# Performance work log

Hardware: AMD Instinct MI355X
Metric: run time of the kernel (lower is better)

## Reference

```python
import jax, jax.numpy as jnp
import numpy as np

DIM = 2560
HEADS = 64
HEAD_DIM = 40
TEMB = 512
FF = 4 * DIM
B = 1
S = 1248
TXT = 224
EPS = 1e-6


def _ln(x, eps=EPS):
    # LayerNorm over last dim, no affine (elementwise_affine=False)
    m = jnp.mean(x, axis=-1, keepdims=True)
    v = jnp.mean(jnp.square(x - m), axis=-1, keepdims=True)
    return (x - m) * jax.lax.rsqrt(v + eps)


def setup_inputs() -> dict:
    key = jax.random.key(0)
    ks = jax.random.split(key, 10)
    w = 0.02
    return {
        "hidden_states": jax.random.normal(ks[0], (B, S, DIM), jnp.float32),
        "emb": jax.random.normal(ks[1], (B, TEMB), jnp.float32),
        "attention_mask": jnp.zeros((B, 1, S, S), jnp.float32),
        "adaln_w": jax.random.normal(ks[2], (TEMB, 12 * DIM), jnp.float32) * w,
        "adaln_b": jnp.zeros((12 * DIM,), jnp.float32),
        "qkv_w": jax.random.normal(ks[3], (DIM, 3 * DIM), jnp.float32) * w,
        "qkv_b": jnp.zeros((3 * DIM,), jnp.float32),
        "out_w": jax.random.normal(ks[4], (DIM, DIM), jnp.float32) * w,
        "out_b": jnp.zeros((DIM,), jnp.float32),
        "ff1_w": jax.random.normal(ks[5], (DIM, FF), jnp.float32) * w,
        "ff1_b": jnp.zeros((FF,), jnp.float32),
        "ff2_w": jax.random.normal(ks[6], (FF, DIM), jnp.float32) * w,
        "ff2_b": jnp.zeros((DIM,), jnp.float32),
        "text_length": TXT,
    }


def reference(hidden_states, emb, attention_mask, adaln_w, adaln_b, qkv_w, qkv_b,
              out_w, out_b, ff1_w, ff1_b, ff2_w, ff2_b, text_length):
    b, s, d = hidden_states.shape
    t = text_length

    # adaLN: SiLU -> Linear(time_embed_dim, 12*dim), chunk into 12 [B, dim] pieces
    ada = jax.nn.silu(emb) @ adaln_w + adaln_b
    (sh_msa_i, sc_msa_i, g_msa_i, sh_mlp_i, sc_mlp_i, g_mlp_i,
     sh_msa_t, sc_msa_t, g_msa_t, sh_mlp_t, sc_mlp_t, g_mlp_t) = jnp.split(ada, 12, axis=1)

    def mod(x, shift, scale):
        return x * (1.0 + scale[:, None, :]) + shift[:, None, :]

    # --- attention block ---
    ai = _ln(hidden_states)
    ai = jnp.concatenate([mod(ai[:, :t], sh_msa_t, sc_msa_t),
                          mod(ai[:, t:], sh_msa_i, sc_msa_i)], axis=1)

    qkv = ai @ qkv_w + qkv_b                              # [B, S, 3*D]
    q, k, v = jnp.split(qkv, 3, axis=-1)
    q = q.reshape(b, s, HEADS, HEAD_DIM).transpose(0, 2, 1, 3)  # [B, H, S, hd]
    k = k.reshape(b, s, HEADS, HEAD_DIM).transpose(0, 2, 1, 3)
    v = v.reshape(b, s, HEADS, HEAD_DIM).transpose(0, 2, 1, 3)

    q = _ln(q)  # per-head QK layernorm
    k = _ln(k)

    scores = jnp.einsum("bhqd,bhkd->bhqk", q, k) / (HEAD_DIM ** 0.5)
    scores = scores + attention_mask
    probs = jax.nn.softmax(scores, axis=-1)
    ctx = jnp.einsum("bhqk,bhkd->bhqd", probs, v)
    ctx = ctx.transpose(0, 2, 1, 3).reshape(b, s, d)
    attn_out = ctx @ out_w + out_b

    h = jnp.concatenate([hidden_states[:, :t] + g_msa_t[:, None, :] * attn_out[:, :t],
                         hidden_states[:, t:] + g_msa_i[:, None, :] * attn_out[:, t:]], axis=1)

    # --- MLP block ---
    mi = _ln(h)
    mi = jnp.concatenate([mod(mi[:, :t], sh_mlp_t, sc_mlp_t),
                          mod(mi[:, t:], sh_mlp_i, sc_mlp_i)], axis=1)
    mo = jax.nn.gelu(mi @ ff1_w + ff1_b, approximate=True) @ ff2_w + ff2_b

    h = jnp.concatenate([h[:, :t] + g_mlp_t[:, None, :] * mo[:, :t],
                         h[:, t:] + g_mlp_i[:, None, :] * mo[:, t:]], axis=1)
    return h
```

## Files before the change

### kernel.cpp

```cpp
#include <hip/hip_runtime.h>
#include <cstdint>

typedef float f32x4 __attribute__((ext_vector_type(4)));
typedef __bf16 bf16x8 __attribute__((ext_vector_type(8)));
typedef __bf16 bf16x4 __attribute__((ext_vector_type(4)));

#define S_LEN 1248
#define S_PAD 1280
#define DIMD 2560
#define NHEAD 64
#define HDIM 40
#define T3 7680

__device__ __forceinline__ f32x4 mfma16(bf16x8 a, bf16x8 b, f32x4 c) {
  return __builtin_amdgcn_mfma_f32_16x16x32_bf16(a, b, c, 0, 0, 0);
}

__global__ void k_adaln(const float* __restrict__ emb, const float* __restrict__ W,
                        const float* __restrict__ b, float* __restrict__ ada) {
  __shared__ __attribute__((aligned(16))) float se[512];
  int tid = threadIdx.x;
  for (int i = tid; i < 512; i += 64) {
    float e = emb[i];
    se[i] = e / (1.f + __expf(-e));
  }
  __syncthreads();
  int col = blockIdx.x * 64 + tid;
  float acc = 0.f;
  #pragma unroll 8
  for (int k = 0; k < 512; ++k) acc += se[k] * W[(size_t)k * 30720 + col];
  ada[col] = acc + b[col];
}

__global__ __launch_bounds__(256) void k_trans(const float* __restrict__ W,
                                               __bf16* __restrict__ Wt, int K, int N) {
  __shared__ __attribute__((aligned(16))) float t[64][65];
  int k0 = blockIdx.y * 64, n0 = blockIdx.x * 64;
  int tid = threadIdx.x;
  #pragma unroll
  for (int i = 0; i < 4; ++i) {
    int r = i * 16 + (tid >> 4), c = (tid & 15) * 4;
    const float4 v = *(const float4*)&W[(size_t)(k0 + r) * N + n0 + c];
    t[r][c] = v.x; t[r][c + 1] = v.y; t[r][c + 2] = v.z; t[r][c + 3] = v.w;
  }
  __syncthreads();
  #pragma unroll
  for (int j = 0; j < 4; ++j) {
    int n = j * 16 + (tid >> 4), kk = (tid & 15) * 4;
    bf16x4 o;
    o[0] = (__bf16)t[kk][n];     o[1] = (__bf16)t[kk + 1][n];
    o[2] = (__bf16)t[kk + 2][n]; o[3] = (__bf16)t[kk + 3][n];
    *(bf16x4*)&Wt[(size_t)(n0 + n) * K + k0 + kk] = o;
  }
}

__global__ __launch_bounds__(256) void k_lnmod(const float* __restrict__ X,
                                               const float* __restrict__ ada,
                                               int csh_t, int csc_t, int csh_i, int csc_i,
                                               const int* __restrict__ tlp,
                                               __bf16* __restrict__ Y) {
  int row = blockIdx.x, tid = threadIdx.x;
  const float* x = X + (size_t)row * DIMD;
  float v[10], s = 0.f, s2 = 0.f;
  #pragma unroll
  for (int i = 0; i < 10; ++i) { v[i] = x[tid + i * 256]; s += v[i]; s2 += v[i] * v[i]; }
  #pragma unroll
  for (int m = 1; m < 64; m <<= 1) { s += __shfl_xor(s, m, 64); s2 += __shfl_xor(s2, m, 64); }
  __shared__ float rs[4], rq[4];
  if ((tid & 63) == 0) { rs[tid >> 6] = s; rq[tid >> 6] = s2; }
  __syncthreads();
  s = rs[0] + rs[1] + rs[2] + rs[3];
  s2 = rq[0] + rq[1] + rq[2] + rq[3];
  float mean = s * (1.f / DIMD);
  float rstd = rsqrtf(s2 * (1.f / DIMD) - mean * mean + 1e-6f);
  int txt = *tlp;
  int csh = row < txt ? csh_t : csh_i, csc = row < txt ? csc_t : csc_i;
  #pragma unroll
  for (int i = 0; i < 10; ++i) {
    int col = tid + i * 256;
    float y = (v[i] - mean) * rstd;
    y = y * (1.f + ada[csc * DIMD + col]) + ada[csh * DIMD + col];
    Y[(size_t)row * DIMD + col] = (__bf16)y;
  }
}

template <int EPI>
__global__ __launch_bounds__(256) void k_gemm(
    const __bf16* __restrict__ A, int lda, const __bf16* __restrict__ Bt, int ldb,
    const float* __restrict__ bias, int N, int ksize,
    float* __restrict__ Cf, float* __restrict__ Cp, __bf16* __restrict__ Cb) {
  __shared__ __attribute__((aligned(16))) __bf16 smem[3][2][4096];
  int tid = threadIdx.x;

  unsigned gx = gridDim.x, gy = gridDim.y;
  unsigned nwg = gx * gy * gridDim.z;
  unsigned orig = (blockIdx.z * gy + blockIdx.y) * gx + blockIdx.x;
  unsigned qq = nwg >> 3, r8 = nwg & 7;
  unsigned xcd = orig & 7, loc = orig >> 3;
  unsigned swz = (xcd < r8 ? xcd * (qq + 1) : r8 * (qq + 1) + (xcd - r8) * qq) + loc;
  unsigned bx = swz % gx;
  unsigned rest = swz / gx;
  unsigned by = rest % gy;
  unsigned bz = rest / gy;

  int m0 = bx * 128, n0 = by * 128;
  int kbase = bz * ksize;
  int wave = tid >> 6, lane = tid & 63;
  int wm = (wave & 1) * 64, wn = (wave >> 1) * 64;
  int l15 = lane & 15, l4 = lane >> 4;
  f32x4 acc[4][4] = {};

  auto STG = [&](__bf16* As, __bf16* Bs, int kk) {
    #pragma unroll
    for (int i = 0; i < 2; ++i) {
      int c = tid + i * 256;
      int row = c >> 2, ko = (c & 3) * 8;
      __builtin_amdgcn_global_load_lds(
          (const __attribute__((address_space(1))) unsigned int*)(A + (size_t)(m0 + row) * lda + kk + ko),
          (__attribute__((address_space(3))) unsigned int*)(As + c * 8), 16, 0, 0);
      __builtin_amdgcn_global_load_lds(
          (const __attribute__((address_space(1))) unsigned int*)(Bt + (size_t)(n0 + row) * ldb + kk + ko),
          (__attribute__((address_space(3))) unsigned int*)(Bs + c * 8), 16, 0, 0);
    }
  };

  int nt = ksize >> 5;
  STG(smem[0][0], smem[0][1], kbase);
  STG(smem[1][0], smem[1][1], kbase + 32);
  asm volatile("s_waitcnt vmcnt(4)" ::: "memory");
  __builtin_amdgcn_s_barrier();

  int rb = 0, sb = 2;
  for (int t = 0; t < nt; ++t) {
    if (t + 2 < nt) STG(smem[sb][0], smem[sb][1], kbase + (t + 2) * 32);
    const __bf16* As = smem[rb][0];
    const __bf16* Bs = smem[rb][1];
    bf16x8 af[4], bfr[4];
    #pragma unroll
    for (int s = 0; s < 4; ++s) {
      af[s] = *(const bf16x8*)&As[(wm + s * 16 + l15) * 32 + l4 * 8];
      bfr[s] = *(const bf16x8*)&Bs[(wn + s * 16 + l15) * 32 + l4 * 8];
    }
    __builtin_amdgcn_s_setprio(1);
    #pragma unroll
    for (int i = 0; i < 4; ++i)
      #pragma unroll
      for (int j = 0; j < 4; ++j)
        acc[i][j] = mfma16(af[i], bfr[j], acc[i][j]);
    __builtin_amdgcn_s_setprio(0);
    __builtin_amdgcn_sched_barrier(0);
    if (t + 2 < nt)
      asm volatile("s_waitcnt vmcnt(4)" ::: "memory");
    else
      asm volatile("s_waitcnt vmcnt(0)" ::: "memory");
    __builtin_amdgcn_s_barrier();
    rb = rb == 2 ? 0 : rb + 1;
    sb = sb == 2 ? 0 : sb + 1;
  }

  float* Cfo = Cf;
  if constexpr (EPI == 3) Cfo = (bz == 0) ? Cf : (Cp + (size_t)(bz - 1) * S_PAD * N);
  #pragma unroll
  for (int i = 0; i < 4; ++i) {
    #pragma unroll
    for (int r = 0; r < 4; ++r) {
      int rr = m0 + wm + i * 16 + l4 * 4 + r;
      if (rr >= S_LEN) continue;
      #pragma unroll
      for (int j = 0; j < 4; ++j) {
        int col = n0 + wn + j * 16 + l15;
        if constexpr (EPI == 0) {
          Cfo[(size_t)rr * N + col] = acc[i][j][r] + bias[col];
        } else if constexpr (EPI == 3) {
          Cfo[(size_t)rr * N + col] = acc[i][j][r];
        } else {
          float val = acc[i][j][r] + bias[col];
          float u = val + 0.044715f * val * val * val;
          float gl = 0.5f * val * (1.f + tanhf(0.7978845608028654f * u));
          Cb[(size_t)rr * N + col] = (__bf16)gl;
        }
      }
    }
  }
}

__global__ __launch_bounds__(256) void k_redq(const float* __restrict__ part,
                                              const float* __restrict__ bias,
                                              float* __restrict__ io) {
  int idx = blockIdx.x * 256 + threadIdx.x;
  int perRow = T3 >> 2;
  int row = idx / perRow;
  int c4 = (idx - row * perRow) << 2;
  size_t off = (size_t)row * T3 + c4;
  const float4 a = *(const float4*)&io[off];
  const float4 p = *(const float4*)&part[off];
  const float4 b = *(const float4*)&bias[c4];
  float4 o;
  o.x = a.x + p.x + b.x; o.y = a.y + p.y + b.y;
  o.z = a.z + p.z + b.z; o.w = a.w + p.w + b.w;
  *(float4*)&io[off] = o;
}

template <int NS>
__global__ __launch_bounds__(256) void k_red(const float* __restrict__ part,
                                             const float* __restrict__ bias,
                                             const float* __restrict__ resid,
                                             const float* __restrict__ ada,
                                             int g_t, int g_i, const int* __restrict__ tlp,
                                             int N, float* __restrict__ out) {
  int idx = blockIdx.x * 256 + threadIdx.x;
  int perRow = N >> 2;
  int row = idx / perRow;
  int c4 = (idx - row * perRow) << 2;
  if (row >= S_LEN) return;
  int txt = *tlp;
  size_t off = (size_t)row * N + c4;
  float4 s = *(const float4*)&part[off];
  #pragma unroll
  for (int z = 1; z < NS; ++z) {
    const float4 p = *(const float4*)&part[(size_t)z * S_PAD * N + off];
    s.x += p.x; s.y += p.y; s.z += p.z; s.w += p.w;
  }
  const float4 bb = *(const float4*)&bias[c4];
  const float4 rr = *(const float4*)&resid[off];
  const float4 gg = *(const float4*)&ada[(size_t)(row < txt ? g_t : g_i) * DIMD + c4];
  float4 o;
  o.x = rr.x + gg.x * (s.x + bb.x);
  o.y = rr.y + gg.y * (s.y + bb.y);
  o.z = rr.z + gg.z * (s.z + bb.z);
  o.w = rr.w + gg.w * (s.w + bb.w);
  *(float4*)&out[off] = o;
}

__global__ __launch_bounds__(128) void k_qkln(const float* __restrict__ qkv,
                                              __bf16* __restrict__ Qb, __bf16* __restrict__ Kb) {
  __shared__ __attribute__((aligned(16))) float buf[5120];
  int srow = blockIdx.x, tid = threadIdx.x;
  const float* rowp = qkv + (size_t)srow * T3;
  for (int i = tid; i < 1280; i += 128)
    *(float4*)&buf[i * 4] = *(const float4*)&rowp[i * 4];
  __syncthreads();
  int h = tid & 63;
  bool isK = tid >= 64;
  const float* x = buf + (isK ? DIMD : 0) + h * HDIM;
  float xv[40], s = 0.f;
  #pragma unroll
  for (int d = 0; d < 40; ++d) { xv[d] = x[d]; s += xv[d]; }
  float mean = s * (1.f / 40.f);
  float s2 = 0.f;
  #pragma unroll
  for (int d = 0; d < 40; ++d) { float t = xv[d] - mean; s2 += t * t; }
  float rstd = rsqrtf(s2 * (1.f / 40.f) + 1e-6f);
  float scale = isK ? rstd : rstd * 0.15811388300841897f;
  __bf16* dst = (isK ? Kb : Qb) + ((size_t)h * S_PAD + srow) * 64;
  #pragma unroll
  for (int i = 0; i < 5; ++i) {
    bf16x8 w;
    #pragma unroll
    for (int j = 0; j < 8; ++j) w[j] = (__bf16)((xv[i * 8 + j] - mean) * scale);
    *(bf16x8*)&dst[i * 8] = w;
  }
  bf16x8 z = {};
  *(bf16x8*)&dst[40] = z;
  *(bf16x8*)&dst[48] = z;
  *(bf16x8*)&dst[56] = z;
}

__global__ __launch_bounds__(256) void k_vtrans(const float* __restrict__ qkv,
                                                __bf16* __restrict__ Vt) {
  __shared__ __attribute__((aligned(16))) float t[64][41];
  int h = blockIdx.y, s0 = blockIdx.x * 64;
  int tid = threadIdx.x;
  for (int i = tid; i < 64 * 40; i += 256) {
    int sr = i / 40, d = i - sr * 40;
    int srow = s0 + sr;
    t[sr][d] = (srow < S_LEN) ? qkv[(size_t)srow * T3 + 2 * DIMD + h * HDIM + d] : 0.f;
  }
  __syncthreads();
  int d = tid >> 2, sc = (tid & 3) * 16;
  bf16x8 w0 = {}, w1 = {};
  if (d < 40) {
    #pragma unroll
    for (int q = 0; q < 8; ++q) {
      w0[q] = (__bf16)t[sc + q][d];
      w1[q] = (__bf16)t[sc + 8 + q][d];
    }
  } else if (d == 40) {
    #pragma unroll
    for (int q = 0; q < 8; ++q) { w0[q] = (__bf16)1.0f; w1[q] = (__bf16)1.0f; }
  }
  __bf16* dst = Vt + ((size_t)h * 64 + d) * S_PAD + s0 + sc;
  *(bf16x8*)&dst[0] = w0;
  *(bf16x8*)&dst[8] = w1;
}

__global__ __launch_bounds__(256) void k_attn(const __bf16* __restrict__ Qb,
                                              const __bf16* __restrict__ Kb,
                                              const __bf16* __restrict__ Vt,
                                              const float* __restrict__ mask,
                                              __bf16* __restrict__ ctx) {
  __shared__ __attribute__((aligned(16))) __bf16 kvs[2][2][4096];
  __shared__ __attribute__((aligned(16))) __bf16 plds[4][2][1024];
  unsigned orig = blockIdx.y * 10 + blockIdx.x;
  unsigned swz = (orig & 7) * 80 + (orig >> 3);
  int h = swz / 10, q0 = (swz % 10) * 128;
  int tid = threadIdx.x, wave = tid >> 6, lane = tid & 63;
  int l15 = lane & 15, l4 = lane >> 4;
  int qb = q0 + wave * 32;

  const __bf16* Kh = Kb + (size_t)h * S_PAD * 64;
  const __bf16* Vh = Vt + (size_t)h * 64 * S_PAD;

  auto STAGE = [&](int buf, int kv0) {
    #pragma unroll
    for (int i = 0; i < 2; ++i) {
      int c = tid + i * 256;
      int row = c >> 3, col = ((c & 7) ^ (row & 7)) * 8;
      __builtin_amdgcn_global_load_lds(
          (const __attribute__((address_space(1))) unsigned int*)(Kh + (size_t)(kv0 + row) * 64 + col),
          (__attribute__((address_space(3))) unsigned int*)&kvs[buf][0][c * 8], 16, 0, 0);
      __builtin_amdgcn_global_load_lds(
          (const __attribute__((address_space(1))) unsigned int*)(Vh + (size_t)row * S_PAD + kv0 + col),
          (__attribute__((address_space(3))) unsigned int*)&kvs[buf][1][c * 8], 16, 0, 0);
    }
  };

  bf16x8 qf[2][2];
  #pragma unroll
  for (int g = 0; g < 2; ++g) {
    const __bf16* Qp = Qb + ((size_t)h * S_PAD + qb + g * 16 + l15) * 64 + l4 * 8;
    qf[g][0] = *(const bf16x8*)Qp;
    qf[g][1] = *(const bf16x8*)(Qp + 32);
  }
  const float* mrow[2][4];
  #pragma unroll
  for (int g = 0; g < 2; ++g)
    #pragma unroll
    for (int r = 0; r < 4; ++r) {
      int qr = qb + g * 16 + l4 * 4 + r;
      mrow[g][r] = mask + (size_t)(qr < S_LEN ? qr : S_LEN - 1) * S_LEN;
    }
  f32x4 o[2][3] = {};

  STAGE(0, 0);
  for (int t = 0; t < 20; ++t) {
    int kv0 = t * 64;
    if (t < 19) {
      STAGE((t + 1) & 1, kv0 + 64);
      asm volatile("s_waitcnt vmcnt(4)" ::: "memory");
    } else {
      asm volatile("s_waitcnt vmcnt(0)" ::: "memory");
    }
    __builtin_amdgcn_s_barrier();
    const __bf16* Ks = kvs[t & 1][0];
    const __bf16* Vs = kvs[t & 1][1];

    float mreg[2][4][4];
    #pragma unroll
    for (int g = 0; g < 2; ++g)
      #pragma unroll
      for (int ns = 0; ns < 4; ++ns) {
        int kvc = kv0 + ns * 16 + l15;
        int mc = kvc < S_LEN ? kvc : S_LEN - 1;
        #pragma unroll
        for (int r = 0; r < 4; ++r) mreg[g][ns][r] = mrow[g][r][mc];
      }

    bf16x8 kf[4][2];
    #pragma unroll
    for (int ns = 0; ns < 4; ++ns) {
      int kvr = ns * 16 + l15, sw = kvr & 7;
      kf[ns][0] = *(const bf16x8*)((const char*)Ks + kvr * 128 + ((l4 ^ sw) << 4));
      kf[ns][1] = *(const bf16x8*)((const char*)Ks + kvr * 128 + (((4 + l4) ^ sw) << 4));
    }
    bf16x8 vf[3][2];
    #pragma unroll
    for (int d3 = 0; d3 < 3; ++d3) {
      int dr = d3 * 16 + l15, sw = dr & 7;
      vf[d3][0] = *(const bf16x8*)((const char*)Vs + dr * 128 + ((l4 ^ sw) << 4));
      vf[d3][1] = *(const bf16x8*)((const char*)Vs + dr * 128 + (((4 + l4) ^ sw) << 4));
    }

    #pragma unroll
    for (int g = 0; g < 2; ++g) {
      f32x4 sf[4];
      #pragma unroll
      for (int ns = 0; ns < 4; ++ns) {
        f32x4 a = {};
        a = mfma16(qf[g][0], kf[ns][0], a);
        a = mfma16(qf[g][1], kf[ns][1], a);
        sf[ns] = a;
      }
      #pragma unroll
      for (int ns = 0; ns < 4; ++ns) {
        int kvc = kv0 + ns * 16 + l15;
        #pragma unroll
        for (int r = 0; r < 4; ++r) {
          float val = sf[ns][r] - 8.f + mreg[g][ns][r];
          if (kvc >= S_LEN) val = -100.f;
          float e = __expf(val);
          int prow = l4 * 4 + r;
          int boff = (prow * 128 + (ns * 16 + l15) * 2) ^ ((prow & 7) << 4);
          plds[wave][g][boff >> 1] = (__bf16)e;
        }
      }
      int swp = (l15 & 7) << 4;
      int ba = l15 * 128 + l4 * 16;
      bf16x8 pa0 = *(const bf16x8*)((const char*)plds[wave][g] + (ba ^ swp));
      bf16x8 pa1 = *(const bf16x8*)((const char*)plds[wave][g] + ((ba + 64) ^ swp));
      #pragma unroll
      for (int d3 = 0; d3 < 3; ++d3) {
        o[g][d3] = mfma16(pa0, vf[d3][0], o[g][d3]);
        o[g][d3] = mfma16(pa1, vf[d3][1], o[g][d3]);
      }
    }
    __builtin_amdgcn_s_barrier();
  }

  #pragma unroll
  for (int g = 0; g < 2; ++g) {
    #pragma unroll
    for (int r = 0; r < 4; ++r) {
      float sum = __shfl(o[g][2][r], (lane & 0x30) + 8, 64);
      float rinv = 1.f / sum;
      int qr = qb + g * 16 + l4 * 4 + r;
      if (qr < S_LEN) {
        #pragma unroll
        for (int d3 = 0; d3 < 3; ++d3) {
          int d = d3 * 16 + l15;
          if (d < HDIM)
            ctx[(size_t)qr * DIMD + h * HDIM + d] = (__bf16)(o[g][d3][r] * rinv);
        }
      }
    }
  }
}

extern "C" void kernel_launch(void* const* d_in, const int* in_sizes, int n_in,
                              void* d_out, int out_size, void* d_ws, size_t ws_size,
                              hipStream_t stream) {
  const float* hidden  = (const float*)d_in[0];
  const float* emb     = (const float*)d_in[1];
  const float* mask    = (const float*)d_in[2];
  const float* adaln_w = (const float*)d_in[3];
  const float* adaln_b = (const float*)d_in[4];
  const float* qkv_w   = (const float*)d_in[5];
  const float* qkv_b   = (const float*)d_in[6];
  const float* out_w   = (const float*)d_in[7];
  const float* out_b   = (const float*)d_in[8];
  const float* ff1_w   = (const float*)d_in[9];
  const float* ff1_b   = (const float*)d_in[10];
  const float* ff2_w   = (const float*)d_in[11];
  const float* ff2_b   = (const float*)d_in[12];
  const int*   tl      = (const int*)d_in[13];
  (void)in_sizes; (void)n_in; (void)out_size; (void)ws_size;

  char* w = (char*)d_ws;
  size_t off = 0;
  auto alloc = [&](size_t b) { char* p = w + off; off += (b + 255) & ~(size_t)255; return p; };
  float*  ada  = (float*)alloc(30720 * 4);
  __bf16* wT   = (__bf16*)alloc((size_t)10240 * 2560 * 2);
  __bf16* ai   = (__bf16*)alloc((size_t)S_PAD * DIMD * 2);
  float*  qkvf = (float*)alloc((size_t)S_PAD * T3 * 4);
  __bf16* Qb   = (__bf16*)alloc((size_t)NHEAD * S_PAD * 64 * 2);
  __bf16* Kb   = (__bf16*)alloc((size_t)NHEAD * S_PAD * 64 * 2);
  __bf16* Vt   = (__bf16*)alloc((size_t)NHEAD * 64 * S_PAD * 2);
  __bf16* ctxb = (__bf16*)alloc((size_t)S_PAD * DIMD * 2);
  float*  hbuf = (float*)alloc((size_t)S_PAD * DIMD * 4);
  __bf16* mi   = ai;
  __bf16* ff1o = (__bf16*)qkvf;
  float* partQ = (float*)Qb;
  float* partO = (float*)qkvf;
  float* partF = (float*)Qb;

  k_adaln<<<dim3(480), dim3(64), 0, stream>>>(emb, adaln_w, adaln_b, ada);
  k_lnmod<<<dim3(1248), dim3(256), 0, stream>>>(hidden, ada, 6, 7, 0, 1, tl, ai);
  k_trans<<<dim3(7680 / 64, 2560 / 64), dim3(256), 0, stream>>>(qkv_w, wT, 2560, 7680);
  k_gemm<3><<<dim3(10, 60, 2), dim3(256), 0, stream>>>(ai, 2560, wT, 2560, nullptr, 7680, 1280,
                                                       qkvf, partQ, nullptr);
  k_redq<<<dim3(9360), dim3(256), 0, stream>>>(partQ, qkv_b, qkvf);
  k_qkln<<<dim3(1248), dim3(128), 0, stream>>>(qkvf, Qb, Kb);
  k_vtrans<<<dim3(20, 64), dim3(256), 0, stream>>>(qkvf, Vt);
  k_attn<<<dim3(10, 64), dim3(256), 0, stream>>>(Qb, Kb, Vt, mask, ctxb);
  k_trans<<<dim3(2560 / 64, 2560 / 64), dim3(256), 0, stream>>>(out_w, wT, 2560, 2560);
  k_gemm<3><<<dim3(10, 20, 4), dim3(256), 0, stream>>>(ctxb, 2560, wT, 2560, nullptr, 2560, 640,
                                                       partO, partO + (size_t)S_PAD * 2560, nullptr);
  k_red<4><<<dim3(3120), dim3(256), 0, stream>>>(partO, out_b, hidden, ada, 8, 2, tl, 2560, hbuf);
  k_lnmod<<<dim3(1248), dim3(256), 0, stream>>>(hbuf, ada, 9, 10, 3, 4, tl, mi);
  k_trans<<<dim3(10240 / 64, 2560 / 64), dim3(256), 0, stream>>>(ff1_w, wT, 2560, 10240);
  k_gemm<2><<<dim3(10, 80, 1), dim3(256), 0, stream>>>(mi, 2560, wT, 2560, ff1_b, 10240, 2560,
                                                       nullptr, nullptr, ff1o);
  k_trans<<<dim3(2560 / 64, 10240 / 64), dim3(256), 0, stream>>>(ff2_w, wT, 10240, 2560);
  k_gemm<3><<<dim3(10, 20, 2), dim3(256), 0, stream>>>(ff1o, 10240, wT, 10240, nullptr, 2560, 5120,
                                                       partF, partF + (size_t)S_PAD * 2560, nullptr);
  k_red<2><<<dim3(3120), dim3(256), 0, stream>>>(partF, ff2_b, hbuf, ada, 11, 5, tl, 2560, (float*)d_out);
}
```

Measured before the change: 572.9 us.

## Split attention KV across two blocks, drop QKV split-K, rebalance FF2 split

Attention now splits the key/value range in two along grid z. Each half writes unnormalized fp32 partial outputs plus its row-sum column, and a new reduction kernel combines the halves, normalizes and writes bf16 context. The QKV GEMM drops split-K and its separate reduction kernel, fusing the bias in the epilogue. FF2 moves from split-2 to split-4, with partials written partly into the output buffer to reuse memory. Combining halves by simply adding sums assumes both halves share the same softmax max reference, which holds only if the kernel uses no running max (e.g. fixed bounded scores via QK layernorm); otherwise this risks wrong results.

After: 590.9 us. 1.03x slower.

```diff
diff --git a/kernel.cpp b/kernel.cpp
--- a/kernel.cpp
+++ b/kernel.cpp
@@ -11,6 +11,7 @@
 #define NHEAD 64
 #define HDIM 40
 #define T3 7680
+#define APSTRIDE 2816
 
 __device__ __forceinline__ f32x4 mfma16(bf16x8 a, bf16x8 b, f32x4 c) {
   return __builtin_amdgcn_mfma_f32_16x16x32_bf16(a, b, c, 0, 0, 0);
@@ -184,25 +185,9 @@
   }
 }
 
-__global__ __launch_bounds__(256) void k_redq(const float* __restrict__ part,
-                                              const float* __restrict__ bias,
-                                              float* __restrict__ io) {
-  int idx = blockIdx.x * 256 + threadIdx.x;
-  int perRow = T3 >> 2;
-  int row = idx / perRow;
-  int c4 = (idx - row * perRow) << 2;
-  size_t off = (size_t)row * T3 + c4;
-  const float4 a = *(const float4*)&io[off];
-  const float4 p = *(const float4*)&part[off];
-  const float4 b = *(const float4*)&bias[c4];
-  float4 o;
-  o.x = a.x + p.x + b.x; o.y = a.y + p.y + b.y;
-  o.z = a.z + p.z + b.z; o.w = a.w + p.w + b.w;
-  *(float4*)&io[off] = o;
-}
-
 template <int NS>
-__global__ __launch_bounds__(256) void k_red(const float* __restrict__ part,
+__global__ __launch_bounds__(256) void k_red(const float* __restrict__ p0,
+                                             const float* __restrict__ prest,
                                              const float* __restrict__ bias,
                                              const float* __restrict__ resid,
                                              const float* __restrict__ ada,
@@ -215,10 +200,10 @@
   if (row >= S_LEN) return;
   int txt = *tlp;
   size_t off = (size_t)row * N + c4;
-  float4 s = *(const float4*)&part[off];
-  #pragma unroll
-  for (int z = 1; z < NS; ++z) {
-    const float4 p = *(const float4*)&part[(size_t)z * S_PAD * N + off];
+  float4 s = *(const float4*)&p0[(size_t)row * N + c4];
+  #pragma unroll
+  for (int z = 0; z < NS - 1; ++z) {
+    const float4 p = *(const float4*)&prest[(size_t)z * S_PAD * N + off];
     s.x += p.x; s.y += p.y; s.z += p.z; s.w += p.w;
   }
   const float4 bb = *(const float4*)&bias[c4];
@@ -298,12 +283,14 @@
                                               const __bf16* __restrict__ Kb,
                                               const __bf16* __restrict__ Vt,
                                               const float* __restrict__ mask,
-                                              __bf16* __restrict__ ctx) {
+                                              float* __restrict__ part) {
   __shared__ __attribute__((aligned(16))) __bf16 kvs[2][2][4096];
   __shared__ __attribute__((aligned(16))) __bf16 plds[4][2][1024];
   unsigned orig = blockIdx.y * 10 + blockIdx.x;
   unsigned swz = (orig & 7) * 80 + (orig >> 3);
   int h = swz / 10, q0 = (swz % 10) * 128;
+  int z = blockIdx.z;
+  int kvbase = z * 640;
   int tid = threadIdx.x, wave = tid >> 6, lane = tid & 63;
   int l15 = lane & 15, l4 = lane >> 4;
   int qb = q0 + wave * 32;
@@ -342,10 +329,10 @@
     }
   f32x4 o[2][3] = {};
 
-  STAGE(0, 0);
-  for (int t = 0; t < 20; ++t) {
-    int kv0 = t * 64;
-    if (t < 19) {
+  STAGE(0, kvbase);
+  for (int t = 0; t < 10; ++t) {
+    int kv0 = kvbase + t * 64;
+    if (t < 9) {
       STAGE((t + 1) & 1, kv0 + 64);
       asm volatile("s_waitcnt vmcnt(4)" ::: "memory");
     } else {
@@ -417,22 +404,41 @@
     __builtin_amdgcn_s_barrier();
   }
 
+  float* pz = part + (size_t)z * S_PAD * APSTRIDE;
   #pragma unroll
   for (int g = 0; g < 2; ++g) {
     #pragma unroll
     for (int r = 0; r < 4; ++r) {
-      float sum = __shfl(o[g][2][r], (lane & 0x30) + 8, 64);
-      float rinv = 1.f / sum;
       int qr = qb + g * 16 + l4 * 4 + r;
-      if (qr < S_LEN) {
-        #pragma unroll
-        for (int d3 = 0; d3 < 3; ++d3) {
-          int d = d3 * 16 + l15;
-          if (d < HDIM)
-            ctx[(size_t)qr * DIMD + h * HDIM + d] = (__bf16)(o[g][d3][r] * rinv);
-        }
+      if (qr >= S_LEN) continue;
+      float* base = pz + (size_t)qr * APSTRIDE + h * 44;
+      #pragma unroll
+      for (int d3 = 0; d3 < 3; ++d3) {
+        int d = d3 * 16 + l15;
+        if (d <= 40) base[d] = o[g][d3][r];
       }
     }
+  }
+}
+
+__global__ __launch_bounds__(256) void k_ared(const float* __restrict__ part,
+                                              __bf16* __restrict__ ctx) {
+  int idx = blockIdx.x * 256 + threadIdx.x;
+  int qr = idx >> 6, h = idx & 63;
+  if (qr >= S_LEN) return;
+  const float* p0 = part + (size_t)qr * APSTRIDE + h * 44;
+  const float* p1 = p0 + (size_t)S_PAD * APSTRIDE;
+  float rinv = 1.f / (p0[40] + p1[40]);
+  __bf16* dst = ctx + (size_t)qr * DIMD + h * HDIM;
+  #pragma unroll
+  for (int i = 0; i < 5; ++i) {
+    bf16x8 w;
+    #pragma unroll
+    for (int j = 0; j < 8; ++j) {
+      int d = i * 8 + j;
+      w[j] = (__bf16)((p0[d] + p1[d]) * rinv);
+    }
+    *(bf16x8*)&dst[i * 8] = w;
   }
 }
 
@@ -467,31 +473,34 @@
   __bf16* Vt   = (__bf16*)alloc((size_t)NHEAD * 64 * S_PAD * 2);
   __bf16* ctxb = (__bf16*)alloc((size_t)S_PAD * DIMD * 2);
   float*  hbuf = (float*)alloc((size_t)S_PAD * DIMD * 4);
-  __bf16* mi   = ai;
-  __bf16* ff1o = (__bf16*)qkvf;
-  float* partQ = (float*)Qb;
-  float* partO = (float*)qkvf;
-  float* partF = (float*)Qb;
+  __bf16* mi    = ai;
+  float*  partA = (float*)qkvf;
+  float*  partO = (float*)qkvf;
+  __bf16* ff1o  = Qb;
+  float*  partF = (float*)qkvf;
+  float*  outf  = (float*)d_out;
 
   k_adaln<<<dim3(480), dim3(64), 0, stream>>>(emb, adaln_w, adaln_b, ada);
   k_lnmod<<<dim3(1248), dim3(256), 0, stream>>>(hidden, ada, 6, 7, 0, 1, tl, ai);
   k_trans<<<dim3(7680 / 64, 2560 / 64), dim3(256), 0, stream>>>(qkv_w, wT, 2560, 7680);
-  k_gemm<3><<<dim3(10, 60, 2), dim3(256), 0, stream>>>(ai, 2560, wT, 2560, nullptr, 7680, 1280,
-                                                       qkvf, partQ, nullptr);
-  k_redq<<<dim3(9360), dim3(256), 0, stream>>>(partQ, qkv_b, qkvf);
+  k_gemm<0><<<dim3(10, 60, 1), dim3(256), 0, stream>>>(ai, 2560, wT, 2560, qkv_b, 7680, 2560,
+                                                       qkvf, nullptr, nullptr);
   k_qkln<<<dim3(1248), dim3(128), 0, stream>>>(qkvf, Qb, Kb);
   k_vtrans<<<dim3(20, 64), dim3(256), 0, stream>>>(qkvf, Vt);
-  k_attn<<<dim3(10, 64), dim3(256), 0, stream>>>(Qb, Kb, Vt, mask, ctxb);
+  k_attn<<<dim3(10, 64, 2), dim3(256), 0, stream>>>(Qb, Kb, Vt, mask, partA);
+  k_ared<<<dim3(312), dim3(256), 0, stream>>>(partA, ctxb);
   k_trans<<<dim3(2560 / 64, 2560 / 64), dim3(256), 0, stream>>>(out_w, wT, 2560, 2560);
   k_gemm<3><<<dim3(10, 20, 4), dim3(256), 0, stream>>>(ctxb, 2560, wT, 2560, nullptr, 2560, 640,
-                                                       partO, partO + (size_t)S_PAD * 2560, nullptr);
-  k_red<4><<<dim3(3120), dim3(256), 0, stream>>>(partO, out_b, hidden, ada, 8, 2, tl, 2560, hbuf);
+                                                       outf, partO, nullptr);
+  k_red<4><<<dim3(3120), dim3(256), 0, stream>>>(outf, partO, out_b, hidden, ada, 8, 2, tl,
+                                                 2560, hbuf);
   k_lnmod<<<dim3(1248), dim3(256), 0, stream>>>(hbuf, ada, 9, 10, 3, 4, tl, mi);
   k_trans<<<dim3(10240 / 64, 2560 / 64), dim3(256), 0, stream>>>(ff1_w, wT, 2560, 10240);
   k_gemm<2><<<dim3(10, 80, 1), dim3(256), 0, stream>>>(mi, 2560, wT, 2560, ff1_b, 10240, 2560,
                                                        nullptr, nullptr, ff1o);
   k_trans<<<dim3(2560 / 64, 10240 / 64), dim3(256), 0, stream>>>(ff2_w, wT, 10240, 2560);
-  k_gemm<3><<<dim3(10, 20, 2), dim3(256), 0, stream>>>(ff1o, 10240, wT, 10240, nullptr, 2560, 5120,
-                                                       partF, partF + (size_t)S_PAD * 2560, nullptr);
-  k_red<2><<<dim3(3120), dim3(256), 0, stream>>>(partF, ff2_b, hbuf, ada, 11, 5, tl, 2560, (float*)d_out);
-}
+  k_gemm<3><<<dim3(10, 20, 4), dim3(256), 0, stream>>>(ff1o, 10240, wT, 10240, nullptr, 2560, 2560,
+                                                       outf, partF, nullptr);
+  k_red<4><<<dim3(3120), dim3(256), 0, stream>>>(outf, partF, ff2_b, hbuf, ada, 11, 5, tl,
+                                                 2560, outf);
+}
```

## Add BM=64 GEMM tile variant, drop QKV split-K, retune split-K factors

Applied to the files above, without the earlier changes.

The GEMM kernel is templated on the M tile size so it can run with 64-row tiles. The QKV and FF1 GEMMs now use BM=64 with twice as many blocks, and QKV no longer uses split-K, which removes the separate k_redq reduction pass and its partial buffer traffic. The out-projection split-K drops from 4 to 2 and FF2 rises from 2 to 4, with the first partial written into the output buffer. Buffers are reassigned to match. The smaller tiles improve occupancy and wave balance across CUs but give less operand reuse per block.

Measured after the change: 659.2 us. +15.1%, slower.

```diff
diff --git a/kernel.cpp b/kernel.cpp
--- a/kernel.cpp
+++ b/kernel.cpp
@@ -84,12 +84,15 @@
   }
 }
 
-template <int EPI>
+template <int BM, int EPI>
 __global__ __launch_bounds__(256) void k_gemm(
     const __bf16* __restrict__ A, int lda, const __bf16* __restrict__ Bt, int ldb,
     const float* __restrict__ bias, int N, int ksize,
     float* __restrict__ Cf, float* __restrict__ Cp, __bf16* __restrict__ Cb) {
-  __shared__ __attribute__((aligned(16))) __bf16 smem[3][2][4096];
+  constexpr int MF = (BM == 128) ? 4 : 2;
+  constexpr int ALOADS = BM / 64;
+  __shared__ __attribute__((aligned(16))) __bf16 smA[3][BM * 32];
+  __shared__ __attribute__((aligned(16))) __bf16 smB[3][128 * 32];
   int tid = threadIdx.x;
 
   unsigned gx = gridDim.x, gy = gridDim.y;
@@ -103,21 +106,26 @@
   unsigned by = rest % gy;
   unsigned bz = rest / gy;
 
-  int m0 = bx * 128, n0 = by * 128;
+  int m0 = bx * BM, n0 = by * 128;
   int kbase = bz * ksize;
   int wave = tid >> 6, lane = tid & 63;
-  int wm = (wave & 1) * 64, wn = (wave >> 1) * 64;
+  int wm = (wave & 1) * (BM / 2), wn = (wave >> 1) * 64;
   int l15 = lane & 15, l4 = lane >> 4;
-  f32x4 acc[4][4] = {};
+  f32x4 acc[MF][4] = {};
 
   auto STG = [&](__bf16* As, __bf16* Bs, int kk) {
     #pragma unroll
-    for (int i = 0; i < 2; ++i) {
+    for (int i = 0; i < ALOADS; ++i) {
       int c = tid + i * 256;
       int row = c >> 2, ko = (c & 3) * 8;
       __builtin_amdgcn_global_load_lds(
           (const __attribute__((address_space(1))) unsigned int*)(A + (size_t)(m0 + row) * lda + kk + ko),
           (__attribute__((address_space(3))) unsigned int*)(As + c * 8), 16, 0, 0);
+    }
+    #pragma unroll
+    for (int i = 0; i < 2; ++i) {
+      int c = tid + i * 256;
+      int row = c >> 2, ko = (c & 3) * 8;
       __builtin_amdgcn_global_load_lds(
           (const __attribute__((address_space(1))) unsigned int*)(Bt + (size_t)(n0 + row) * ldb + kk + ko),
           (__attribute__((address_space(3))) unsigned int*)(Bs + c * 8), 16, 0, 0);
@@ -125,34 +133,38 @@
   };
 
   int nt = ksize >> 5;
-  STG(smem[0][0], smem[0][1], kbase);
-  STG(smem[1][0], smem[1][1], kbase + 32);
-  asm volatile("s_waitcnt vmcnt(4)" ::: "memory");
+  STG(smA[0], smB[0], kbase);
+  STG(smA[1], smB[1], kbase + 32);
+  if constexpr (BM == 128) asm volatile("s_waitcnt vmcnt(4)" ::: "memory");
+  else                     asm volatile("s_waitcnt vmcnt(3)" ::: "memory");
   __builtin_amdgcn_s_barrier();
 
   int rb = 0, sb = 2;
   for (int t = 0; t < nt; ++t) {
-    if (t + 2 < nt) STG(smem[sb][0], smem[sb][1], kbase + (t + 2) * 32);
-    const __bf16* As = smem[rb][0];
-    const __bf16* Bs = smem[rb][1];
-    bf16x8 af[4], bfr[4];
-    #pragma unroll
-    for (int s = 0; s < 4; ++s) {
+    if (t + 2 < nt) STG(smA[sb], smB[sb], kbase + (t + 2) * 32);
+    const __bf16* As = smA[rb];
+    const __bf16* Bs = smB[rb];
+    bf16x8 af[MF], bfr[4];
+    #pragma unroll
+    for (int s = 0; s < MF; ++s)
       af[s] = *(const bf16x8*)&As[(wm + s * 16 + l15) * 32 + l4 * 8];
+    #pragma unroll
+    for (int s = 0; s < 4; ++s)
       bfr[s] = *(const bf16x8*)&Bs[(wn + s * 16 + l15) * 32 + l4 * 8];
-    }
     __builtin_amdgcn_s_setprio(1);
     #pragma unroll
-    for (int i = 0; i < 4; ++i)
+    for (int i = 0; i < MF; ++i)
       #pragma unroll
       for (int j = 0; j < 4; ++j)
         acc[i][j] = mfma16(af[i], bfr[j], acc[i][j]);
     __builtin_amdgcn_s_setprio(0);
     __builtin_amdgcn_sched_barrier(0);
-    if (t + 2 < nt)
-      asm volatile("s_waitcnt vmcnt(4)" ::: "memory");
-    else
+    if (t + 2 < nt) {
+      if constexpr (BM == 128) asm volatile("s_waitcnt vmcnt(4)" ::: "memory");
+      else                     asm volatile("s_waitcnt vmcnt(3)" ::: "memory");
+    } else {
       asm volatile("s_waitcnt vmcnt(0)" ::: "memory");
+    }
     __builtin_amdgcn_s_barrier();
     rb = rb == 2 ? 0 : rb + 1;
     sb = sb == 2 ? 0 : sb + 1;
@@ -161,7 +173,7 @@
   float* Cfo = Cf;
   if constexpr (EPI == 3) Cfo = (bz == 0) ? Cf : (Cp + (size_t)(bz - 1) * S_PAD * N);
   #pragma unroll
-  for (int i = 0; i < 4; ++i) {
+  for (int i = 0; i < MF; ++i) {
     #pragma unroll
     for (int r = 0; r < 4; ++r) {
       int rr = m0 + wm + i * 16 + l4 * 4 + r;
@@ -184,25 +196,9 @@
   }
 }
 
-__global__ __launch_bounds__(256) void k_redq(const float* __restrict__ part,
-                                              const float* __restrict__ bias,
-                                              float* __restrict__ io) {
-  int idx = blockIdx.x * 256 + threadIdx.x;
-  int perRow = T3 >> 2;
-  int row = idx / perRow;
-  int c4 = (idx - row * perRow) << 2;
-  size_t off = (size_t)row * T3 + c4;
-  const float4 a = *(const float4*)&io[off];
-  const float4 p = *(const float4*)&part[off];
-  const float4 b = *(const float4*)&bias[c4];
-  float4 o;
-  o.x = a.x + p.x + b.x; o.y = a.y + p.y + b.y;
-  o.z = a.z + p.z + b.z; o.w = a.w + p.w + b.w;
-  *(float4*)&io[off] = o;
-}
-
 template <int NS>
-__global__ __launch_bounds__(256) void k_red(const float* __restrict__ part,
+__global__ __launch_bounds__(256) void k_red(const float* __restrict__ p0,
+                                             const float* __restrict__ prest,
                                              const float* __restrict__ bias,
                                              const float* __restrict__ resid,
                                              const float* __restrict__ ada,
@@ -215,10 +211,10 @@
   if (row >= S_LEN) return;
   int txt = *tlp;
   size_t off = (size_t)row * N + c4;
-  float4 s = *(const float4*)&part[off];
-  #pragma unroll
-  for (int z = 1; z < NS; ++z) {
-    const float4 p = *(const float4*)&part[(size_t)z * S_PAD * N + off];
+  float4 s = *(const float4*)&p0[off];
+  #pragma unroll
+  for (int z = 0; z < NS - 1; ++z) {
+    const float4 p = *(const float4*)&prest[(size_t)z * S_PAD * N + off];
     s.x += p.x; s.y += p.y; s.z += p.z; s.w += p.w;
   }
   const float4 bb = *(const float4*)&bias[c4];
@@ -467,31 +463,32 @@
   __bf16* Vt   = (__bf16*)alloc((size_t)NHEAD * 64 * S_PAD * 2);
   __bf16* ctxb = (__bf16*)alloc((size_t)S_PAD * DIMD * 2);
   float*  hbuf = (float*)alloc((size_t)S_PAD * DIMD * 4);
-  __bf16* mi   = ai;
-  __bf16* ff1o = (__bf16*)qkvf;
-  float* partQ = (float*)Qb;
-  float* partO = (float*)qkvf;
-  float* partF = (float*)Qb;
+  __bf16* mi    = ai;
+  float*  partO = (float*)Qb;
+  __bf16* ff1o  = Qb;
+  float*  partF = (float*)qkvf;
+  float*  outf  = (float*)d_out;
 
   k_adaln<<<dim3(480), dim3(64), 0, stream>>>(emb, adaln_w, adaln_b, ada);
   k_lnmod<<<dim3(1248), dim3(256), 0, stream>>>(hidden, ada, 6, 7, 0, 1, tl, ai);
   k_trans<<<dim3(7680 / 64, 2560 / 64), dim3(256), 0, stream>>>(qkv_w, wT, 2560, 7680);
-  k_gemm<3><<<dim3(10, 60, 2), dim3(256), 0, stream>>>(ai, 2560, wT, 2560, nullptr, 7680, 1280,
-                                                       qkvf, partQ, nullptr);
-  k_redq<<<dim3(9360), dim3(256), 0, stream>>>(partQ, qkv_b, qkvf);
+  k_gemm<64, 0><<<dim3(20, 60, 1), dim3(256), 0, stream>>>(ai, 2560, wT, 2560, qkv_b, 7680, 2560,
+                                                           qkvf, nullptr, nullptr);
   k_qkln<<<dim3(1248), dim3(128), 0, stream>>>(qkvf, Qb, Kb);
   k_vtrans<<<dim3(20, 64), dim3(256), 0, stream>>>(qkvf, Vt);
   k_attn<<<dim3(10, 64), dim3(256), 0, stream>>>(Qb, Kb, Vt, mask, ctxb);
   k_trans<<<dim3(2560 / 64, 2560 / 64), dim3(256), 0, stream>>>(out_w, wT, 2560, 2560);
-  k_gemm<3><<<dim3(10, 20, 4), dim3(256), 0, stream>>>(ctxb, 2560, wT, 2560, nullptr, 2560, 640,
-                                                       partO, partO + (size_t)S_PAD * 2560, nullptr);
-  k_red<4><<<dim3(3120), dim3(256), 0, stream>>>(partO, out_b, hidden, ada, 8, 2, tl, 2560, hbuf);
+  k_gemm<128, 3><<<dim3(10, 20, 2), dim3(256), 0, stream>>>(ctxb, 2560, wT, 2560, nullptr, 2560, 1280,
+                                                            partO, partO + (size_t)S_PAD * 2560, nullptr);
+  k_red<2><<<dim3(3120), dim3(256), 0, stream>>>(partO, partO + (size_t)S_PAD * 2560, out_b,
+                                                 hidden, ada, 8, 2, tl, 2560, hbuf);
   k_lnmod<<<dim3(1248), dim3(256), 0, stream>>>(hbuf, ada, 9, 10, 3, 4, tl, mi);
   k_trans<<<dim3(10240 / 64, 2560 / 64), dim3(256), 0, stream>>>(ff1_w, wT, 2560, 10240);
-  k_gemm<2><<<dim3(10, 80, 1), dim3(256), 0, stream>>>(mi, 2560, wT, 2560, ff1_b, 10240, 2560,
-                                                       nullptr, nullptr, ff1o);
+  k_gemm<64, 2><<<dim3(20, 80, 1), dim3(256), 0, stream>>>(mi, 2560, wT, 2560, ff1_b, 10240, 2560,
+                                                           nullptr, nullptr, ff1o);
   k_trans<<<dim3(2560 / 64, 10240 / 64), dim3(256), 0, stream>>>(ff2_w, wT, 10240, 2560);
-  k_gemm<3><<<dim3(10, 20, 2), dim3(256), 0, stream>>>(ff1o, 10240, wT, 10240, nullptr, 2560, 5120,
-                                                       partF, partF + (size_t)S_PAD * 2560, nullptr);
-  k_red<2><<<dim3(3120), dim3(256), 0, stream>>>(partF, ff2_b, hbuf, ada, 11, 5, tl, 2560, (float*)d_out);
-}
+  k_gemm<128, 3><<<dim3(10, 20, 4), dim3(256), 0, stream>>>(ff1o, 10240, wT, 10240, nullptr, 2560, 2560,
+                                                            outf, partF, nullptr);
+  k_red<4><<<dim3(3120), dim3(256), 0, stream>>>(outf, partF, ff2_b, hbuf, ada, 11, 5, tl,
+                                                 2560, outf);
+}
```
